# Kernel optimization log

Hardware: AMD Instinct MI355X
Metric: run time of the kernel (lower is better)

## Reference

```python
import jax, jax.numpy as jnp
import numpy as np

B, N, T, F_IN, H, OUT = 64, 207, 48, 6, 64, 1
RANK = 24  # fixed inner dim of learned adjacency factors


def setup_inputs() -> dict:
    key = jax.random.key(0)
    ks = jax.random.split(key, 10)
    s = lambda k, shp, sc=1.0: jax.random.normal(k, shp, jnp.float32) * sc
    return {
        "x": s(ks[0], (B, N, T, F_IN)),
        "N1": s(ks[1], (N, RANK)),
        "N2": s(ks[2], (RANK, N)),
        "W1": s(ks[3], (F_IN, H), 0.2),
        "b1": jnp.zeros((H,), jnp.float32),
        "W2": s(ks[4], (H, H), 0.1),
        "b2": jnp.zeros((H,), jnp.float32),
        "W_ih": s(ks[5], (4 * H, H), 0.1),
        "W_hh": s(ks[6], (4 * H, H), 0.1),
        "b_ih": jnp.zeros((4 * H,), jnp.float32),
        "b_hh": jnp.zeros((4 * H,), jnp.float32),
        "W_fc": s(ks[7], (H, OUT), 0.1),
        "b_fc": jnp.zeros((OUT,), jnp.float32),
    }


def reference(x, N1, N2, W1, b1, W2, b2, W_ih, W_hh, b_ih, b_hh, W_fc, b_fc):
    Bn, Nn, Tn, Fn = x.shape
    # sigmoid(N1@N2) > 0 everywhere -> dense_to_sparse yields ALL N^2 edges
    # (self-loops included); GCNConv's gcn_norm adds one extra self-loop,
    # edge weights all 1 -> A = ones + I, deg = N+1, symmetric normalization.
    adj = jax.nn.sigmoid(N1 @ N2)
    mask = (adj > 0).astype(x.dtype)  # structurally all-ones
    A = mask + jnp.eye(Nn, dtype=x.dtype)
    dinv = jax.lax.rsqrt(A.sum(axis=1))
    A_hat = dinv[:, None] * A * dinv[None, :]  # [N, N]

    xt = jnp.transpose(x, (0, 2, 1, 3))  # [B, T, N, F]
    # GCNConv: propagate(x @ W) with sym-norm, then bias; relu; dropout=eval no-op
    h = jax.nn.relu(jnp.einsum('mn,btnh->btmh', A_hat, xt @ W1) + b1)
    h = jax.nn.relu(jnp.einsum('mn,btnh->btmh', A_hat, h @ W2) + b2)

    # [B, T, N, H] -> [B*N, T, H] for the LSTM
    seq = jnp.transpose(h, (0, 2, 1, 3)).reshape(Bn * Nn, Tn, -1)
    Hd = W_hh.shape[1]

    def step(carry, x_t):
        h_prev, c_prev = carry
        g = x_t @ W_ih.T + b_ih + h_prev @ W_hh.T + b_hh
        i, f, gg, o = jnp.split(g, 4, axis=-1)  # torch gate order i,f,g,o
        c = jax.nn.sigmoid(f) * c_prev + jax.nn.sigmoid(i) * jnp.tanh(gg)
        h_new = jax.nn.sigmoid(o) * jnp.tanh(c)
        return (h_new, c), None

    h0 = jnp.zeros((Bn * Nn, Hd), x.dtype)
    (hT, _), _ = jax.lax.scan(step, (h0, h0), jnp.transpose(seq, (1, 0, 2)))
    out = hT @ W_fc + b_fc  # [B*N, OUT]
    return out.reshape(Bn, Nn, -1)
```

## Files before the change

kernel.cpp:

```cpp
#include <hip/hip_runtime.h>
#include <math.h>

#define NB 64
#define NN 207
#define NT 48
#define NF 6
#define NH 64
#define NSEQ (NB*NN)
#define NG   (NSEQ/16)
#define TSU  ((size_t)NSEQ*NH)

typedef short bf8_t __attribute__((ext_vector_type(8)));
typedef float f4_t  __attribute__((ext_vector_type(4)));
typedef unsigned short ushort;
typedef unsigned int uint;

__device__ __forceinline__ ushort bf16h(float x){
  uint u = __float_as_uint(x);
  return (ushort)((u + 0x7FFF + ((u>>16)&1)) >> 16);
}
__device__ __forceinline__ float bf16f(ushort h){
  return __uint_as_float((uint)h << 16);
}
__device__ __forceinline__ float fsig(float x){
  return __builtin_amdgcn_rcpf(1.0f + __expf(-x));
}
__device__ __forceinline__ float ftanh(float x){
  x = fminf(15.0f, fmaxf(-15.0f, x));
  float e = __expf(2.0f*x);
  return 1.0f - 2.0f*__builtin_amdgcn_rcpf(e + 1.0f);
}


#define HW 72
#define XS6 40
#define GCN7_LDS_BYTES (208*HW*2 + (207*XS6 + NF*64 + 64 + 64 + 6*64 + 6*64 + 48)*4)

__global__ __launch_bounds__(256, 2) void gcn_kernel(
    const float* __restrict__ x, const float* __restrict__ W1, const float* __restrict__ b1,
    const float* __restrict__ W2, const float* __restrict__ b2,
    ushort* __restrict__ sxh, ushort* __restrict__ sxl)
{
  extern __shared__ char smraw[];
  ushort* h1b = (ushort*)smraw;
  float*  xs6 = (float*)(h1b + 208*HW);
  float*  W1s = xs6 + 207*XS6;
  float*  b1s = W1s + NF*64;
  float*  b2s = b1s + 64;
  float*  S2_ = b2s + 64;
  float*  r1_ = S2_ + 6*64;
  float*  xsA = r1_ + 6*64;

  const int tid = threadIdx.x;
  const int tg = blockIdx.x, b = blockIdx.y;
  const float inv = 1.0f/208.0f;
  const int l = tid & 63;
  const int w = __builtin_amdgcn_readfirstlane(tid >> 6);
  const int col = l & 15, q = l >> 4;
  const int cw = w*16 + col;

  for (int i=tid; i<6*64; i+=256){ S2_[i]=0.f; r1_[i]=0.f; }
  if (tid < 48) xsA[tid] = 0.f;
  if (tid < 72) h1b[207*HW + tid] = 0;

  for (int i=tid;i<NF*64;i+=256) W1s[i]=W1[i];
  if (tid<64){ b1s[tid]=b1[tid]; b2s[tid]=b2[tid]; }
  {
    const float* xb = x + (size_t)b*NN*(NT*NF) + (size_t)tg*36;
    for (int i=tid; i<207*9; i+=256){
      int n = i/9, c = (i - n*9)*4;
      *(float4*)&xs6[n*XS6 + c] = *(const float4*)&xb[(size_t)n*(NT*NF) + c];
    }
  }
  __syncthreads();

  if (tid < 144){
    int tt = tid/24, rem = tid - tt*24, f = rem>>2, p = rem&3;
    float ps = 0.f;
    for (int n=p; n<NN; n+=4) ps += xs6[n*XS6 + tt*6 + f];
    atomicAdd(&xsA[tt*8+f], ps);
  }

  float wtmp[16];
  #pragma unroll
  for (int kc=0;kc<2;kc++)
    #pragma unroll
    for (int j=0;j<8;j++)
      wtmp[kc*8+j] = W2[(size_t)(kc*32 + q*8 + j)*64 + cw];
  bf8_t B2[2];
  #pragma unroll
  for (int kc=0;kc<2;kc++){
    bf8_t ph;
    #pragma unroll
    for (int j=0;j<8;j++) ph[j] = (short)bf16h(wtmp[kc*8+j]);
    B2[kc]=ph;
  }
  __syncthreads();

  const int ht4 = (tid & 15) * 4;
  const int nti = tid >> 4;

  #pragma unroll 1
  for (int tt=0; tt<6; tt++){
    const int t = tg*6 + tt;
    {
      float s1v[4];
      #pragma unroll
      for (int j=0;j<4;j++){
        float a = 0.f;
        #pragma unroll
        for (int f=0;f<NF;f++) a += xsA[tt*8+f]*W1s[f*64 + ht4 + j];
        s1v[j] = a;
      }
      float cs0=0.f, cs1=0.f, cs2=0.f, cs3=0.f;
      #pragma unroll 1
      for (int p=0;p<4;p++){
        int nt = p*16 + nti;
        if (nt < 52){
          #pragma unroll
          for (int i=0;i<4;i++){
            int n = 4*nt+i;
            if (n < NN){
              float a0=0.f,a1=0.f,a2=0.f,a3=0.f;
              #pragma unroll
              for (int f=0;f<NF;f++){
                float xv = xs6[n*XS6 + tt*6 + f];
                float4 wv = *(const float4*)&W1s[f*64 + ht4];
                a0+=xv*wv.x; a1+=xv*wv.y; a2+=xv*wv.z; a3+=xv*wv.w;
              }
              float v0=(a0+s1v[0])*inv + b1s[ht4+0]; v0 = v0>0.f?v0:0.f;
              float v1=(a1+s1v[1])*inv + b1s[ht4+1]; v1 = v1>0.f?v1:0.f;
              float v2=(a2+s1v[2])*inv + b1s[ht4+2]; v2 = v2>0.f?v2:0.f;
              float v3=(a3+s1v[3])*inv + b1s[ht4+3]; v3 = v3>0.f?v3:0.f;
              ushort4 hi;
              hi.x=bf16h(v0); hi.y=bf16h(v1); hi.z=bf16h(v2); hi.w=bf16h(v3);
              *(ushort4*)&h1b[n*HW + ht4] = hi;
              cs0+=v0; cs1+=v1; cs2+=v2; cs3+=v3;
            }
          }
        }
      }
      atomicAdd(&r1_[tt*64+ht4+0], cs0);
      atomicAdd(&r1_[tt*64+ht4+1], cs1);
      atomicAdd(&r1_[tt*64+ht4+2], cs2);
      atomicAdd(&r1_[tt*64+ht4+3], cs3);
    }
    __syncthreads();

    {
      int h = tid & 63, pp = tid >> 6;
      float ps = 0.f;
      #pragma unroll
      for (int k=0;k<16;k++) ps += r1_[tt*64+pp*16+k]*W2[(size_t)(pp*16+k)*64 + h];
      atomicAdd(&S2_[tt*64+h], ps);
    }

    f4_t acc[13];
    #pragma unroll
    for (int mt=0;mt<13;mt++){ f4_t z; z[0]=0.f;z[1]=0.f;z[2]=0.f;z[3]=0.f; acc[mt]=z; }
    #pragma unroll 2
    for (int mt=0;mt<13;mt++){
      #pragma unroll
      for (int kc=0;kc<2;kc++){
        bf8_t ah = *(const bf8_t*)(h1b + (mt*16+col)*HW + kc*32 + q*8);
        acc[mt] = __builtin_amdgcn_mfma_f32_16x16x32_bf16(ah, B2[kc], acc[mt], 0,0,0);
      }
    }
    __syncthreads();

    {
      const float s2v = S2_[tt*64+cw], b2v = b2s[cw];
      const size_t obase = (size_t)t*TSU + (size_t)(b*NN)*NH + cw;
      #pragma unroll
      for (int mt=0;mt<13;mt++){
        #pragma unroll
        for (int r=0;r<4;r++){
          int n = mt*16 + q*4 + r;
          if (n < NN){
            float v = (acc[mt][r] + s2v)*inv + b2v;
            v = v>0.f ? v : 0.f;
            ushort hb = bf16h(v);
            sxh[obase + (size_t)n*NH] = hb;
            sxl[obase + (size_t)n*NH] = bf16h(v - bf16f(hb));
          }
        }
      }
    }
  }
}

#define HS 68

__global__ __launch_bounds__(256, 2) void lstm15_kernel(
    const ushort* __restrict__ sxh, const ushort* __restrict__ sxl,
    const float* __restrict__ Wih, const float* __restrict__ Whh,
    const float* __restrict__ bih, const float* __restrict__ bhh,
    const float* __restrict__ Wfc, const float* __restrict__ bfc, float* __restrict__ out)
{
  __shared__ uint hf[2][16*HS + 4];

  const int tid = threadIdx.x;
  const int l = tid & 63;
  const int w = __builtin_amdgcn_readfirstlane(tid >> 6);
  const int col = l & 15, q = l >> 4;
  const int g = blockIdx.x;

  bf8_t Bh[4][4], Bl[4][4];
  #pragma unroll
  for (int mat=0; mat<2; mat++){
    const float* W = mat ? Whh : Wih;
    #pragma unroll
    for (int ty=0; ty<4; ty++){
      #pragma unroll
      for (int kk=0; kk<2; kk++){
        const float* wp = W + (size_t)(ty*64 + w*16 + col)*64 + kk*32 + q*8;
        bf8_t ph, pl;
        #pragma unroll
        for (int j=0;j<8;j++){
          float wv = wp[j];
          ushort hb = bf16h(wv);
          ph[j] = (short)hb;
          pl[j] = (short)bf16h(wv - bf16f(hb));
        }
        Bh[ty][mat*2+kk] = ph;
        Bl[ty][mat*2+kk] = pl;
      }
    }
  }
  float bias[4];
  #pragma unroll
  for (int ty=0;ty<4;ty++){
    int r = ty*64 + w*16 + col;
    bias[ty] = bih[r] + bhh[r];
  }
  float c[4];
  #pragma unroll
  for (int i=0;i<4;i++) c[i]=0.f;

  for (int i=tid; i<16*HS; i+=256) hf[0][i] = 0;

  const ushort* xgh = sxh + (size_t)g*1024 + (size_t)(col*64 + q*8);
  const ushort* xgl = sxl + (size_t)g*1024 + (size_t)(col*64 + q*8);

  bf8_t pxh[2][2], pxl[2][2];
  #pragma unroll
  for (int s2=0; s2<2; s2++){
    const size_t off = (size_t)s2*TSU;
    pxh[s2][0] = *(const bf8_t*)(xgh + off);
    pxh[s2][1] = *(const bf8_t*)(xgh + off + 32);
    pxl[s2][0] = *(const bf8_t*)(xgl + off);
    pxl[s2][1] = *(const bf8_t*)(xgl + off + 32);
  }

  const int d = w*16 + col;
  const uint* hrd = &hf[0][0] + col*HS + q*8;
  __syncthreads();

  #pragma unroll 2
  for (int t=0; t<NT; t++){
    const int cur = t & 1;
    bf8_t cxh0 = pxh[cur][0], cxh1 = pxh[cur][1];
    bf8_t cxl0 = pxl[cur][0], cxl1 = pxl[cur][1];
    if (t+2 < NT){
      const size_t off = (size_t)(t+2)*TSU;
      pxh[cur][0] = *(const bf8_t*)(xgh + off);
      pxh[cur][1] = *(const bf8_t*)(xgh + off + 32);
      pxl[cur][0] = *(const bf8_t*)(xgl + off);
      pxl[cur][1] = *(const bf8_t*)(xgl + off + 32);
    }

    bf8_t hh[2], hl[2];
    {
      const uint* hb = hrd + (cur ? (16*HS+4) : 0);
      uint4 h0 = *(const uint4*)(hb);
      uint4 h1 = *(const uint4*)(hb + 4);
      uint4 h2 = *(const uint4*)(hb + 32);
      uint4 h3 = *(const uint4*)(hb + 36);
      uint u[8];
      u[0]=h0.x;u[1]=h0.y;u[2]=h0.z;u[3]=h0.w;u[4]=h1.x;u[5]=h1.y;u[6]=h1.z;u[7]=h1.w;
      #pragma unroll
      for (int j=0;j<8;j++){ hh[0][j]=(short)(u[j]>>16); hl[0][j]=(short)(u[j]&0xffff); }
      u[0]=h2.x;u[1]=h2.y;u[2]=h2.z;u[3]=h2.w;u[4]=h3.x;u[5]=h3.y;u[6]=h3.z;u[7]=h3.w;
      #pragma unroll
      for (int j=0;j<8;j++){ hh[1][j]=(short)(u[j]>>16); hl[1][j]=(short)(u[j]&0xffff); }
    }

    f4_t acc[4];
    #pragma unroll
    for (int ty=0;ty<4;ty++){ f4_t z; z[0]=bias[ty];z[1]=bias[ty];z[2]=bias[ty];z[3]=bias[ty]; acc[ty]=z; }
    #pragma unroll
    for (int ty=0;ty<4;ty++){
      acc[ty] = __builtin_amdgcn_mfma_f32_16x16x32_bf16(cxh0,  Bh[ty][0], acc[ty], 0,0,0);
      acc[ty] = __builtin_amdgcn_mfma_f32_16x16x32_bf16(cxl0,  Bh[ty][0], acc[ty], 0,0,0);
      acc[ty] = __builtin_amdgcn_mfma_f32_16x16x32_bf16(cxh0,  Bl[ty][0], acc[ty], 0,0,0);
      acc[ty] = __builtin_amdgcn_mfma_f32_16x16x32_bf16(cxh1,  Bh[ty][1], acc[ty], 0,0,0);
      acc[ty] = __builtin_amdgcn_mfma_f32_16x16x32_bf16(cxl1,  Bh[ty][1], acc[ty], 0,0,0);
      acc[ty] = __builtin_amdgcn_mfma_f32_16x16x32_bf16(cxh1,  Bl[ty][1], acc[ty], 0,0,0);
      acc[ty] = __builtin_amdgcn_mfma_f32_16x16x32_bf16(hh[0], Bh[ty][2], acc[ty], 0,0,0);
      acc[ty] = __builtin_amdgcn_mfma_f32_16x16x32_bf16(hl[0], Bh[ty][2], acc[ty], 0,0,0);
      acc[ty] = __builtin_amdgcn_mfma_f32_16x16x32_bf16(hh[0], Bl[ty][2], acc[ty], 0,0,0);
      acc[ty] = __builtin_amdgcn_mfma_f32_16x16x32_bf16(hh[1], Bh[ty][3], acc[ty], 0,0,0);
      acc[ty] = __builtin_amdgcn_mfma_f32_16x16x32_bf16(hl[1], Bh[ty][3], acc[ty], 0,0,0);
      acc[ty] = __builtin_amdgcn_mfma_f32_16x16x32_bf16(hh[1], Bl[ty][3], acc[ty], 0,0,0);
    }

    {
      uint* hw = &hf[cur^1][0];
      #pragma unroll
      for (int r=0;r<4;r++){
        float ig = fsig(acc[0][r]);
        float fg = fsig(acc[1][r]);
        float gt = ftanh(acc[2][r]);
        float og = fsig(acc[3][r]);
        float cc = fg*c[r] + ig*gt;
        c[r] = cc;
        float hv = og*ftanh(cc);
        int off = (q*4+r)*HS + d;
        if (t != NT-1){
          ushort hb2 = bf16h(hv);
          ushort lb2 = bf16h(hv - bf16f(hb2));
          hw[off] = ((uint)hb2<<16) | (uint)lb2;
        } else {
          hw[off] = __float_as_uint(hv);
        }
      }
    }
    __syncthreads();
  }

  if (tid < 16){
    float a = bfc[0];
    const uint* hT = &hf[NT&1][0];
    #pragma unroll 8
    for (int k=0;k<64;k++) a += __uint_as_float(hT[tid*HS + k]) * Wfc[k];
    out[g*16 + tid] = a;
  }
}

extern "C" void kernel_launch(void* const* d_in, const int* in_sizes, int n_in,
                              void* d_out, int out_size, void* d_ws, size_t ws_size,
                              hipStream_t stream) {
  const float* x   = (const float*)d_in[0];
  const float* W1  = (const float*)d_in[3];
  const float* b1  = (const float*)d_in[4];
  const float* W2  = (const float*)d_in[5];
  const float* b2  = (const float*)d_in[6];
  const float* Wih = (const float*)d_in[7];
  const float* Whh = (const float*)d_in[8];
  const float* bih = (const float*)d_in[9];
  const float* bhh = (const float*)d_in[10];
  const float* Wfc = (const float*)d_in[11];
  const float* bfc = (const float*)d_in[12];

  ushort* sxh = (ushort*)d_ws;
  ushort* sxl = sxh + (size_t)NT*TSU;
  float*  out = (float*)d_out;

  hipFuncSetAttribute((const void*)gcn_kernel, hipFuncAttributeMaxDynamicSharedMemorySize, GCN7_LDS_BYTES);

  gcn_kernel<<<dim3(NT/6, NB), 256, GCN7_LDS_BYTES, stream>>>(x, W1, b1, W2, b2, sxh, sxl);
  lstm15_kernel<<<NG, 256, 0, stream>>>(sxh, sxl, Wih, Whh, bih, bhh, Wfc, bfc, out);
}
```

Before: 333.9 us.

## Overlap input-projection MFMAs with barrier and split h LDS into hi/lo planes

Moves the barrier so the input-side MFMAs for step t run before waiting on the previous step's hidden state, hiding the barrier and LDS latency behind x-projection work. The hidden state is now stored in separate bf16 hi and lo LDS arrays with padded stride, so each lane reads ready-made bf8 vectors instead of unpacking interleaved uint words. Hardware packed bf16 conversion replaces the manual rounding. This costs more narrow 16-bit LDS stores and relies on a sched_barrier to hold the instruction order.

```diff
diff --git a/kernel.cpp b/kernel.cpp
--- a/kernel.cpp
+++ b/kernel.cpp
@@ -189,15 +189,16 @@
   }
 }
 
-#define HS 68
-
-__global__ __launch_bounds__(256, 2) void lstm15_kernel(
+#define HS2 72
+
+__global__ __launch_bounds__(256, 2) void lstm16_kernel(
     const ushort* __restrict__ sxh, const ushort* __restrict__ sxl,
     const float* __restrict__ Wih, const float* __restrict__ Whh,
     const float* __restrict__ bih, const float* __restrict__ bhh,
     const float* __restrict__ Wfc, const float* __restrict__ bfc, float* __restrict__ out)
 {
-  __shared__ uint hf[2][16*HS + 4];
+  __shared__ __align__(16) ushort hhp[2][16*HS2 + 8];
+  __shared__ __align__(16) ushort hlp[2][16*HS2 + 8];
 
   const int tid = threadIdx.x;
   const int l = tid & 63;
@@ -237,7 +238,7 @@
   #pragma unroll
   for (int i=0;i<4;i++) c[i]=0.f;
 
-  for (int i=tid; i<16*HS; i+=256) hf[0][i] = 0;
+  for (int i=tid; i<16*HS2; i+=256){ hhp[0][i] = 0; hlp[0][i] = 0; }
 
   const ushort* xgh = sxh + (size_t)g*1024 + (size_t)(col*64 + q*8);
   const ushort* xgl = sxl + (size_t)g*1024 + (size_t)(col*64 + q*8);
@@ -253,7 +254,6 @@
   }
 
   const int d = w*16 + col;
-  const uint* hrd = &hf[0][0] + col*HS + q*8;
   __syncthreads();
 
   #pragma unroll 2
@@ -269,43 +269,45 @@
       pxl[cur][1] = *(const bf8_t*)(xgl + off + 32);
     }
 
-    bf8_t hh[2], hl[2];
-    {
-      const uint* hb = hrd + (cur ? (16*HS+4) : 0);
-      uint4 h0 = *(const uint4*)(hb);
-      uint4 h1 = *(const uint4*)(hb + 4);
-      uint4 h2 = *(const uint4*)(hb + 32);
-      uint4 h3 = *(const uint4*)(hb + 36);
-      uint u[8];
-      u[0]=h0.x;u[1]=h0.y;u[2]=h0.z;u[3]=h0.w;u[4]=h1.x;u[5]=h1.y;u[6]=h1.z;u[7]=h1.w;
-      #pragma unroll
-      for (int j=0;j<8;j++){ hh[0][j]=(short)(u[j]>>16); hl[0][j]=(short)(u[j]&0xffff); }
-      u[0]=h2.x;u[1]=h2.y;u[2]=h2.z;u[3]=h2.w;u[4]=h3.x;u[5]=h3.y;u[6]=h3.z;u[7]=h3.w;
-      #pragma unroll
-      for (int j=0;j<8;j++){ hh[1][j]=(short)(u[j]>>16); hl[1][j]=(short)(u[j]&0xffff); }
-    }
-
     f4_t acc[4];
     #pragma unroll
     for (int ty=0;ty<4;ty++){ f4_t z; z[0]=bias[ty];z[1]=bias[ty];z[2]=bias[ty];z[3]=bias[ty]; acc[ty]=z; }
     #pragma unroll
     for (int ty=0;ty<4;ty++){
-      acc[ty] = __builtin_amdgcn_mfma_f32_16x16x32_bf16(cxh0,  Bh[ty][0], acc[ty], 0,0,0);
-      acc[ty] = __builtin_amdgcn_mfma_f32_16x16x32_bf16(cxl0,  Bh[ty][0], acc[ty], 0,0,0);
-      acc[ty] = __builtin_amdgcn_mfma_f32_16x16x32_bf16(cxh0,  Bl[ty][0], acc[ty], 0,0,0);
-      acc[ty] = __builtin_amdgcn_mfma_f32_16x16x32_bf16(cxh1,  Bh[ty][1], acc[ty], 0,0,0);
-      acc[ty] = __builtin_amdgcn_mfma_f32_16x16x32_bf16(cxl1,  Bh[ty][1], acc[ty], 0,0,0);
-      acc[ty] = __builtin_amdgcn_mfma_f32_16x16x32_bf16(cxh1,  Bl[ty][1], acc[ty], 0,0,0);
-      acc[ty] = __builtin_amdgcn_mfma_f32_16x16x32_bf16(hh[0], Bh[ty][2], acc[ty], 0,0,0);
-      acc[ty] = __builtin_amdgcn_mfma_f32_16x16x32_bf16(hl[0], Bh[ty][2], acc[ty], 0,0,0);
-      acc[ty] = __builtin_amdgcn_mfma_f32_16x16x32_bf16(hh[0], Bl[ty][2], acc[ty], 0,0,0);
-      acc[ty] = __builtin_amdgcn_mfma_f32_16x16x32_bf16(hh[1], Bh[ty][3], acc[ty], 0,0,0);
-      acc[ty] = __builtin_amdgcn_mfma_f32_16x16x32_bf16(hl[1], Bh[ty][3], acc[ty], 0,0,0);
-      acc[ty] = __builtin_amdgcn_mfma_f32_16x16x32_bf16(hh[1], Bl[ty][3], acc[ty], 0,0,0);
-    }
-
-    {
-      uint* hw = &hf[cur^1][0];
+      acc[ty] = __builtin_amdgcn_mfma_f32_16x16x32_bf16(cxh0, Bh[ty][0], acc[ty], 0,0,0);
+      acc[ty] = __builtin_amdgcn_mfma_f32_16x16x32_bf16(cxl0, Bh[ty][0], acc[ty], 0,0,0);
+      acc[ty] = __builtin_amdgcn_mfma_f32_16x16x32_bf16(cxh0, Bl[ty][0], acc[ty], 0,0,0);
+      acc[ty] = __builtin_amdgcn_mfma_f32_16x16x32_bf16(cxh1, Bh[ty][1], acc[ty], 0,0,0);
+      acc[ty] = __builtin_amdgcn_mfma_f32_16x16x32_bf16(cxl1, Bh[ty][1], acc[ty], 0,0,0);
+      acc[ty] = __builtin_amdgcn_mfma_f32_16x16x32_bf16(cxh1, Bl[ty][1], acc[ty], 0,0,0);
+    }
+    __builtin_amdgcn_sched_barrier(0);
+
+    __syncthreads();
+
+    bf8_t hh0, hh1, hl0, hl1;
+    {
+      const ushort* ph = &hhp[cur][0] + col*HS2 + q*8;
+      const ushort* pl = &hlp[cur][0] + col*HS2 + q*8;
+      hh0 = *(const bf8_t*)(ph);
+      hh1 = *(const bf8_t*)(ph + 32);
+      hl0 = *(const bf8_t*)(pl);
+      hl1 = *(const bf8_t*)(pl + 32);
+    }
+    #pragma unroll
+    for (int ty=0;ty<4;ty++){
+      acc[ty] = __builtin_amdgcn_mfma_f32_16x16x32_bf16(hh0, Bh[ty][2], acc[ty], 0,0,0);
+      acc[ty] = __builtin_amdgcn_mfma_f32_16x16x32_bf16(hl0, Bh[ty][2], acc[ty], 0,0,0);
+      acc[ty] = __builtin_amdgcn_mfma_f32_16x16x32_bf16(hh0, Bl[ty][2], acc[ty], 0,0,0);
+      acc[ty] = __builtin_amdgcn_mfma_f32_16x16x32_bf16(hh1, Bh[ty][3], acc[ty], 0,0,0);
+      acc[ty] = __builtin_amdgcn_mfma_f32_16x16x32_bf16(hl1, Bh[ty][3], acc[ty], 0,0,0);
+      acc[ty] = __builtin_amdgcn_mfma_f32_16x16x32_bf16(hh1, Bl[ty][3], acc[ty], 0,0,0);
+    }
+
+    {
+      ushort* wh = &hhp[cur^1][0];
+      ushort* wl = &hlp[cur^1][0];
+      float hv[4];
       #pragma unroll
       for (int r=0;r<4;r++){
         float ig = fsig(acc[0][r]);
@@ -314,25 +316,48 @@
         float og = fsig(acc[3][r]);
         float cc = fg*c[r] + ig*gt;
         c[r] = cc;
-        float hv = og*ftanh(cc);
-        int off = (q*4+r)*HS + d;
-        if (t != NT-1){
-          ushort hb2 = bf16h(hv);
-          ushort lb2 = bf16h(hv - bf16f(hb2));
-          hw[off] = ((uint)hb2<<16) | (uint)lb2;
-        } else {
-          hw[off] = __float_as_uint(hv);
+        hv[r] = og*ftanh(cc);
+      }
+      const int o0 = (q*4)*HS2 + d;
+      if (t != NT-1){
+        uint ph01, ph23, pl01, pl23;
+        asm("v_cvt_pk_bf16_f32 %0, %1, %2" : "=v"(ph01) : "v"(hv[0]), "v"(hv[1]));
+        asm("v_cvt_pk_bf16_f32 %0, %1, %2" : "=v"(ph23) : "v"(hv[2]), "v"(hv[3]));
+        float r0 = hv[0] - __uint_as_float(ph01 << 16);
+        float r1 = hv[1] - __uint_as_float(ph01 & 0xffff0000u);
+        float r2 = hv[2] - __uint_as_float(ph23 << 16);
+        float r3 = hv[3] - __uint_as_float(ph23 & 0xffff0000u);
+        asm("v_cvt_pk_bf16_f32 %0, %1, %2" : "=v"(pl01) : "v"(r0), "v"(r1));
+        asm("v_cvt_pk_bf16_f32 %0, %1, %2" : "=v"(pl23) : "v"(r2), "v"(r3));
+        wh[o0]         = (ushort)ph01;
+        wh[o0 + HS2]   = (ushort)(ph01 >> 16);
+        wh[o0 + 2*HS2] = (ushort)ph23;
+        wh[o0 + 3*HS2] = (ushort)(ph23 >> 16);
+        wl[o0]         = (ushort)pl01;
+        wl[o0 + HS2]   = (ushort)(pl01 >> 16);
+        wl[o0 + 2*HS2] = (ushort)pl23;
+        wl[o0 + 3*HS2] = (ushort)(pl23 >> 16);
+      } else {
+        #pragma unroll
+        for (int r=0;r<4;r++){
+          uint bits = __float_as_uint(hv[r]);
+          wh[o0 + r*HS2] = (ushort)(bits >> 16);
+          wl[o0 + r*HS2] = (ushort)(bits & 0xffffu);
         }
       }
     }
-    __syncthreads();
-  }
+  }
+  __syncthreads();
 
   if (tid < 16){
     float a = bfc[0];
-    const uint* hT = &hf[NT&1][0];
+    const ushort* fh = &hhp[NT&1][0] + tid*HS2;
+    const ushort* fl = &hlp[NT&1][0] + tid*HS2;
     #pragma unroll 8
-    for (int k=0;k<64;k++) a += __uint_as_float(hT[tid*HS + k]) * Wfc[k];
+    for (int k=0;k<64;k++){
+      float v = __uint_as_float(((uint)fh[k] << 16) | (uint)fl[k]);
+      a += v * Wfc[k];
+    }
     out[g*16 + tid] = a;
   }
 }
@@ -359,5 +384,5 @@
   hipFuncSetAttribute((const void*)gcn_kernel, hipFuncAttributeMaxDynamicSharedMemorySize, GCN7_LDS_BYTES);
 
   gcn_kernel<<<dim3(NT/6, NB), 256, GCN7_LDS_BYTES, stream>>>(x, W1, b1, W2, b2, sxh, sxl);
-  lstm15_kernel<<<NG, 256, 0, stream>>>(sxh, sxl, Wih, Whh, bih, bhh, Wfc, bfc, out);
-}
+  lstm16_kernel<<<NG, 256, 0, stream>>>(sxh, sxl, Wih, Whh, bih, bhh, Wfc, bfc, out);
+}
```

Result: faster. 320.8 us (-3.9%).
